# Performance work log

Measured on AMD Instinct MI355X. Metric: run time of the kernel, lower is better.

The kernel has to match this reference:

```python
import jax, jax.numpy as jnp
import numpy as np
import math

L, D, H, B, NT = 4, 512, 8, 128, 512
D_HID = int(D * 4.0 / 3.0)  # 682; linear0 outputs 2*D_HID for reglu
EPS = 1e-5


def layer_norm(x, g, b):
    mu = jnp.mean(x, axis=-1, keepdims=True)
    var = jnp.var(x, axis=-1, keepdims=True)
    return (x - mu) * jax.lax.rsqrt(var + EPS) * g + b


def mha(x_q, x_kv, Wq, bq, Wk, bk, Wv, bv, Wo, bo):
    q = x_q @ Wq.T + bq
    k = x_kv @ Wk.T + bk
    v = x_kv @ Wv.T + bv
    Bq, Sq, _ = q.shape
    Sk = k.shape[1]
    dh = D // H
    q = q.reshape(Bq, Sq, H, dh).transpose(0, 2, 1, 3)  # [B,H,Sq,dh]
    k = k.reshape(Bq, Sk, H, dh).transpose(0, 2, 1, 3)
    v = v.reshape(Bq, Sk, H, dh).transpose(0, 2, 1, 3)
    dots = jnp.einsum('bhqd,bhkd->bhqk', q, k) / math.sqrt(dh)
    attn = jax.nn.softmax(dots, axis=-1)
    o = jnp.einsum('bhqk,bhkd->bhqd', attn, v)
    o = o.transpose(0, 2, 1, 3).reshape(Bq, Sq, D)
    return o @ Wo.T + bo


def reglu(x):
    a, b = jnp.split(x, 2, axis=-1)
    return a * jax.nn.relu(b)


def setup_inputs() -> dict:
    key = jax.random.key(0)
    ks = iter(jax.random.split(key, 32))
    s = 0.02
    return {
        'x_num': jax.random.normal(next(ks), (B, NT, D), jnp.float32),
        'cls_w': jax.random.normal(next(ks), (1, D), jnp.float32) * s,
        'Wq': jax.random.normal(next(ks), (L, D, D), jnp.float32) * s,
        'bq': jnp.zeros((L, D), jnp.float32),
        'Wk': jax.random.normal(next(ks), (L, D, D), jnp.float32) * s,
        'bk': jnp.zeros((L, D), jnp.float32),
        'Wv': jax.random.normal(next(ks), (L, D, D), jnp.float32) * s,
        'bv': jnp.zeros((L, D), jnp.float32),
        'Wo': jax.random.normal(next(ks), (L, D, D), jnp.float32) * s,
        'bo': jnp.zeros((L, D), jnp.float32),
        'l0_w': jax.random.normal(next(ks), (L, 2 * D_HID, D), jnp.float32) * s,
        'l0_b': jnp.zeros((L, 2 * D_HID), jnp.float32),
        'l1_w': jax.random.normal(next(ks), (L, D, D_HID), jnp.float32) * s,
        'l1_b': jnp.zeros((L, D), jnp.float32),
        'n0_g': jnp.ones((L - 1, D), jnp.float32),
        'n0_b': jnp.zeros((L - 1, D), jnp.float32),
        'n1_g': jnp.ones((L, D), jnp.float32),
        'n1_b': jnp.zeros((L, D), jnp.float32),
        'ln_g': jnp.ones((D,), jnp.float32),
        'ln_b': jnp.zeros((D,), jnp.float32),
        'head_w': jax.random.normal(next(ks), (1, D), jnp.float32) * s,
        'head_b': jnp.zeros((1,), jnp.float32),
    }


def reference(x_num, cls_w, Wq, bq, Wk, bk, Wv, bv, Wo, bo,
              l0_w, l0_b, l1_w, l1_b, n0_g, n0_b, n1_g, n1_b,
              ln_g, ln_b, head_w, head_b):
    # prepend CLS token: cls_weight broadcast over batch
    x_cls = jnp.broadcast_to(cls_w[None], (x_num.shape[0], 1, D))
    x = jnp.concatenate([x_cls, x_num], axis=1)  # [B, NT+1, D]
    for i in range(L):
        is_last = i + 1 == L
        # attention block (prenormalization; layer 0 has no norm0)
        xr = layer_norm(x, n0_g[i - 1], n0_b[i - 1]) if i > 0 else x
        x_q = xr[:, :1] if is_last else xr  # last layer: query only CLS
        xr = mha(x_q, xr, Wq[i], bq[i], Wk[i], bk[i], Wv[i], bv[i], Wo[i], bo[i])
        if is_last:
            x = x[:, :1]
        x = x + xr
        # FFN block with reglu
        xr = layer_norm(x, n1_g[i], n1_b[i])
        xr = reglu(xr @ l0_w[i].T + l0_b[i])
        xr = xr @ l1_w[i].T + l1_b[i]
        x = x + xr
    x = x[:, 0]  # CLS representation [B, D]
    x = layer_norm(x, ln_g, ln_b)
    x = jax.nn.relu(x)
    x = x @ head_w.T + head_b
    return x.squeeze(-1)  # [B]
```

## Files before the change

kernel.cpp:

```cpp
#include <hip/hip_runtime.h>
#include <stdint.h>

typedef __attribute__((ext_vector_type(4))) float f32x4;
typedef __attribute__((ext_vector_type(8))) short short8;
typedef __attribute__((ext_vector_type(8))) _Float16 half8;

#define DMODEL 512
#define SEQ 513
#define BATCH 128
#define NROWS (BATCH*SEQ)
#define DHID 682
#define DHID2 1364
#define HP 768
#define KTRIM 704
#define QKVS 1536
#define KVB 64
#define NKT8 8
#define QSF 0.1803368801111244f

__device__ __forceinline__ float h2f(ushort u){ return (float)__builtin_bit_cast(_Float16, u); }
__device__ __forceinline__ ushort f2h(float f){ return __builtin_bit_cast(ushort, (_Float16)f); }
__device__ __forceinline__ uint pk2h(float a, float b){
  return __builtin_bit_cast(uint, __builtin_amdgcn_cvt_pkrtz(a, b));
}
__device__ __forceinline__ void gload16(const void* g, void* lds){
  __builtin_amdgcn_global_load_lds((const __attribute__((address_space(1))) void*)g,
                                   (__attribute__((address_space(3))) void*)lds, 16, 0, 0);
}
__device__ __forceinline__ int xcd_wg(int orig, int nwg){
  const int q = nwg >> 3, r = nwg & 7;
  const int xcd = orig & 7, idx = orig >> 3;
  return (xcd < r) ? (xcd*(q+1) + idx) : (r*(q+1) + (xcd-r)*q + idx);
}

template<int EPI>
__global__ __launch_bounds__(256,3) void gemm_bt(
    const ushort* __restrict__ A, const ushort* __restrict__ W,
    const float* __restrict__ bias, ushort* __restrict__ Cb, float* __restrict__ Cf,
    int K, int ldc, int gx, int nwg)
{
  __shared__ char lds[32768];
  const int t = threadIdx.x, lane = t & 63, w = t >> 6;
  const int fr = lane & 15, g = lane >> 4;
  const int l7 = lane & 7, l8 = lane >> 3;
  const int wg = xcd_wg(blockIdx.x, nwg);
  const int row0 = (wg / gx) << 7;
  const int col0 = (wg % gx) << 7;
  const int wr = (w >> 1) << 6, wc = (w & 1) << 6;

  const int chunkoff = (l7 ^ l8) << 3;
  const ushort* Ag = A + (size_t)(row0 + w*8 + l8) * K + chunkoff;
  const ushort* Wg = W + (size_t)(col0 + w*8 + l8) * K + chunkoff;

  f32x4 acc[4][4] = {};

  for (int k0 = 0; k0 < K; k0 += 64) {
    __syncthreads();
#pragma unroll
    for (int p = 0; p < 4; ++p) {
      gload16(Ag + (size_t)(p*32)*K + k0, lds + p*4096 + w*1024);
      gload16(Wg + (size_t)(p*32)*K + k0, lds + 16384 + p*4096 + w*1024);
    }
    __syncthreads();
#pragma unroll
    for (int ks = 0; ks < 2; ++ks) {
      half8 af[4], wf[4];
#pragma unroll
      for (int m = 0; m < 4; ++m) {
        const int row = wr + m*16 + fr;
        af[m] = *(const half8*)(lds + row*128 + (((g + ks*4) ^ (fr & 7)) << 4));
      }
#pragma unroll
      for (int n = 0; n < 4; ++n) {
        const int row = wc + n*16 + fr;
        wf[n] = *(const half8*)(lds + 16384 + row*128 + (((g + ks*4) ^ (fr & 7)) << 4));
      }
#pragma unroll
      for (int m = 0; m < 4; ++m)
#pragma unroll
        for (int n = 0; n < 4; ++n)
          acc[m][n] = __builtin_amdgcn_mfma_f32_16x16x32_f16(af[m], wf[n], acc[m][n], 0, 0, 0);
    }
  }

  const int r0 = (lane >> 4) << 2;
#pragma unroll
  for (int m = 0; m < 4; ++m) {
    const int rg = row0 + wr + m*16 + r0;
#pragma unroll
    for (int n = 0; n < 4; ++n) {
      const int cg = col0 + wc + n*16 + fr;
      const float bi = bias[cg];
      if (EPI == 0) {
#pragma unroll
        for (int r = 0; r < 4; ++r)
          Cb[(size_t)(rg + r)*ldc + cg] = f2h(acc[m][n][r] + bi);
      } else {
#pragma unroll
        for (int r = 0; r < 4; ++r) {
          const size_t ix = (size_t)(rg + r)*ldc + cg;
          Cf[ix] += acc[m][n][r] + bi;
        }
      }
    }
  }
}

template<int XW>
__global__ __launch_bounds__(256,2) void gemm_res_ln(
    const ushort* __restrict__ A, const ushort* __restrict__ W,
    const float* __restrict__ bias, float* __restrict__ x,
    const float* __restrict__ gamma, const float* __restrict__ beta,
    ushort* __restrict__ xb, int K, int lda)
{
  __shared__ char lds[73728];
  const int t = threadIdx.x, lane = t & 63, w = t >> 6;
  const int fr = lane & 15, g = lane >> 4;
  const int l7 = lane & 7, l8 = lane >> 3;
  const int row0 = blockIdx.x << 6;

  const int chunkoff = (l7 ^ l8) << 3;
  const ushort* Ag = A + (size_t)(row0 + w*8 + l8) * lda + chunkoff;
  const ushort* Wg = W + (size_t)(w*8 + l8) * lda + chunkoff;

  f32x4 acc[4][8] = {};

  for (int k0 = 0; k0 < K; k0 += 64) {
    __syncthreads();
    gload16(Ag + k0,                   lds + w*1024);
    gload16(Ag + (size_t)32*lda + k0,  lds + 4096 + w*1024);
#pragma unroll
    for (int p = 0; p < 16; ++p)
      gload16(Wg + (size_t)(p*32)*lda + k0, lds + 8192 + p*4096 + w*1024);
    __syncthreads();
#pragma unroll
    for (int ks = 0; ks < 2; ++ks) {
      half8 af[4], wf[8];
#pragma unroll
      for (int m = 0; m < 4; ++m) {
        const int row = m*16 + fr;
        af[m] = *(const half8*)(lds + row*128 + (((g + ks*4) ^ (fr & 7)) << 4));
      }
#pragma unroll
      for (int n = 0; n < 8; ++n) {
        const int row = (w << 7) + n*16 + fr;
        wf[n] = *(const half8*)(lds + 8192 + row*128 + (((g + ks*4) ^ (fr & 7)) << 4));
      }
#pragma unroll
      for (int m = 0; m < 4; ++m)
#pragma unroll
        for (int n = 0; n < 8; ++n)
          acc[m][n] = __builtin_amdgcn_mfma_f32_16x16x32_f16(af[m], wf[n], acc[m][n], 0, 0, 0);
    }
  }

  ushort* fb16   = (ushort*)lds;
  float2* redrow = (float2*)(lds + 66560);
  float*  gb     = (float*)(lds + 67072);

  __syncthreads();
#pragma unroll
  for (int n = 0; n < 8; ++n) {
    const int cg = (w << 7) + n*16 + fr;
    const float bi = bias[cg];
#pragma unroll
    for (int m = 0; m < 4; ++m)
#pragma unroll
      for (int r = 0; r < 4; ++r)
        fb16[(m*16 + g*4 + r)*520 + cg] = f2h(acc[m][n][r] + bi);
  }
  if (t < 128) *(f32x4*)&gb[t*4]            = *(const f32x4*)&gamma[t*4];
  else         *(f32x4*)&gb[512 + (t-128)*4] = *(const f32x4*)&beta[(t-128)*4];
  __syncthreads();

  const int q = t & 15;
  const int rbase = t >> 4;
#pragma unroll
  for (int rr = 0; rr < 4; ++rr) {
    const int row = rr*16 + rbase;
    const int grow = row0 + row;
    const bool wrx = XW || (grow % SEQ) == 0;
    const size_t xrow = (size_t)grow*DMODEL;
    float ps = 0.f, pss = 0.f;
#pragma unroll
    for (int j = 0; j < 8; ++j) {
      const int c = q*4 + j*64;
      const uint2 pk = *(const uint2*)&fb16[row*520 + c];
      f32x4 v;
      v[0] = h2f((ushort)(pk.x & 0xffffu)); v[1] = h2f((ushort)(pk.x >> 16));
      v[2] = h2f((ushort)(pk.y & 0xffffu)); v[3] = h2f((ushort)(pk.y >> 16));
      const f32x4 xo = *(const f32x4*)&x[xrow + c];
      v += xo;
      if (wrx) *(f32x4*)&x[xrow + c] = v;
      uint2 opk; opk.x = pk2h(v[0], v[1]); opk.y = pk2h(v[2], v[3]);
      *(uint2*)&fb16[row*520 + c] = opk;
      ps  += v[0]+v[1]+v[2]+v[3];
      pss += v[0]*v[0]+v[1]*v[1]+v[2]*v[2]+v[3]*v[3];
    }
#pragma unroll
    for (int mask = 1; mask <= 8; mask <<= 1) {
      ps  += __shfl_xor(ps,  mask);
      pss += __shfl_xor(pss, mask);
    }
    if (q == 0) redrow[row] = float2{ps, pss};
  }
  __syncthreads();
#pragma unroll
  for (int rr = 0; rr < 4; ++rr) {
    const int row = rr*16 + rbase;
    const float2 sr = redrow[row];
    const float mu = sr.x * (1.f/512.f);
    const float rstd = rsqrtf(sr.y*(1.f/512.f) - mu*mu + 1e-5f);
    const size_t xbrow = (size_t)(row0 + row)*DMODEL;
#pragma unroll
    for (int j = 0; j < 8; ++j) {
      const int c = q*4 + j*64;
      const uint2 pk = *(const uint2*)&fb16[row*520 + c];
      f32x4 v;
      v[0] = h2f((ushort)(pk.x & 0xffffu)); v[1] = h2f((ushort)(pk.x >> 16));
      v[2] = h2f((ushort)(pk.y & 0xffffu)); v[3] = h2f((ushort)(pk.y >> 16));
      const f32x4 ga = *(const f32x4*)&gb[c];
      const f32x4 be = *(const f32x4*)&gb[512 + c];
      f32x4 o_;
#pragma unroll
      for (int e = 0; e < 4; ++e) o_[e] = (v[e] - mu)*rstd*ga[e] + be[e];
      uint2 u; u.x = pk2h(o_[0], o_[1]); u.y = pk2h(o_[2], o_[3]);
      *(uint2*)&xb[xbrow + c] = u;
    }
  }
}

__global__ __launch_bounds__(256,2) void gemm_ffn(
    const ushort* __restrict__ A, const ushort* __restrict__ Wa, const ushort* __restrict__ Wb,
    const float* __restrict__ ba, const float* __restrict__ bb, ushort* __restrict__ H,
    int K, int ldc, int gx, int nwg)
{
  __shared__ char lds[49152];
  const int t = threadIdx.x, lane = t & 63, w = t >> 6;
  const int fr = lane & 15, g = lane >> 4;
  const int l7 = lane & 7, l8 = lane >> 3;
  const int wg = xcd_wg(blockIdx.x, nwg);
  const int row0 = (wg / gx) << 7;
  const int col0 = (wg % gx) << 7;
  const int wr = (w >> 1) << 6, wc = (w & 1) << 6;

  const int chunkoff = (l7 ^ l8) << 3;
  const ushort* Ag  = A  + (size_t)(row0 + w*8 + l8) * K + chunkoff;
  const ushort* WaG = Wa + (size_t)(col0 + w*8 + l8) * K + chunkoff;
  const ushort* WbG = Wb + (size_t)(col0 + w*8 + l8) * K + chunkoff;

  f32x4 aa[4][4] = {}, ab[4][4] = {};

  for (int k0 = 0; k0 < K; k0 += 64) {
    __syncthreads();
#pragma unroll
    for (int p = 0; p < 4; ++p) {
      gload16(Ag  + (size_t)(p*32)*K + k0, lds + p*4096 + w*1024);
      gload16(WaG + (size_t)(p*32)*K + k0, lds + 16384 + p*4096 + w*1024);
      gload16(WbG + (size_t)(p*32)*K + k0, lds + 32768 + p*4096 + w*1024);
    }
    __syncthreads();
#pragma unroll
    for (int ks = 0; ks < 2; ++ks) {
      half8 af[4], wa[4], wb[4];
#pragma unroll
      for (int m = 0; m < 4; ++m) {
        const int row = wr + m*16 + fr;
        af[m] = *(const half8*)(lds + row*128 + (((g + ks*4) ^ (fr & 7)) << 4));
      }
#pragma unroll
      for (int n = 0; n < 4; ++n) {
        const int row = wc + n*16 + fr;
        const int off = row*128 + (((g + ks*4) ^ (fr & 7)) << 4);
        wa[n] = *(const half8*)(lds + 16384 + off);
        wb[n] = *(const half8*)(lds + 32768 + off);
      }
#pragma unroll
      for (int m = 0; m < 4; ++m)
#pragma unroll
        for (int n = 0; n < 4; ++n) {
          aa[m][n] = __builtin_amdgcn_mfma_f32_16x16x32_f16(af[m], wa[n], aa[m][n], 0, 0, 0);
          ab[m][n] = __builtin_amdgcn_mfma_f32_16x16x32_f16(af[m], wb[n], ab[m][n], 0, 0, 0);
        }
    }
  }

  const int r0 = (lane >> 4) << 2;
#pragma unroll
  for (int m = 0; m < 4; ++m) {
    const int rg = row0 + wr + m*16 + r0;
#pragma unroll
    for (int n = 0; n < 4; ++n) {
      const int cg = col0 + wc + n*16 + fr;
      const float bav = ba[cg], bbv = bb[cg];
#pragma unroll
      for (int r = 0; r < 4; ++r) {
        const float av = aa[m][n][r] + bav;
        const float bv = ab[m][n][r] + bbv;
        H[(size_t)(rg + r)*ldc + cg] = f2h(av * fmaxf(bv, 0.f));
      }
    }
  }
}

__global__ __launch_bounds__(256,4) void attn_fused(
    const ushort* __restrict__ qkv, ushort* __restrict__ o)
{
  __shared__ char lds[40960];
  const int t = threadIdx.x;

  if (blockIdx.x >= 4096) {
    const int bh = blockIdx.x - 4096;
    const int b = bh >> 3, h = bh & 7;
    float* sc   = (float*)lds;
    float* qsh  = (float*)(lds + 2112);
    float* red  = (float*)(lds + 2368);
    float* osum = (float*)(lds + 2432);
    const ushort* k = qkv + 512;
    const ushort* v = qkv + 1024;
    const ushort* qb2 = qkv + (size_t)512*QKVS;
    if (t < 64) qsh[t] = h2f(qb2[(size_t)b*SEQ*QKVS + h*64 + t]);
    __syncthreads();
    for (int key = t; key < SEQ; key += 256) {
      const ushort* kr = k + ((size_t)b*SEQ + key)*QKVS + h*64;
      float s = 0.f;
#pragma unroll
      for (int dv = 0; dv < 8; ++dv) {
        const short8 kv = *(const short8*)(kr + dv*8);
#pragma unroll
        for (int j = 0; j < 8; ++j) s += qsh[dv*8 + j] * h2f((ushort)kv[j]);
      }
      sc[key] = s;
    }
    __syncthreads();
    float lm = -1e30f;
    for (int key = t; key < SEQ; key += 256) lm = fmaxf(lm, sc[key]);
#pragma unroll
    for (int mask=1; mask<64; mask<<=1) lm = fmaxf(lm, __shfl_xor(lm, mask));
    if ((t&63)==0) red[t>>6] = lm;
    __syncthreads();
    const float mx = fmaxf(fmaxf(red[0],red[1]), fmaxf(red[2],red[3]));
    float ls = 0.f;
    for (int key = t; key < SEQ; key += 256){ float pp = exp2f(sc[key]-mx); sc[key]=pp; ls += pp; }
#pragma unroll
    for (int mask=1; mask<64; mask<<=1) ls += __shfl_xor(ls, mask);
    if ((t&63)==0) red[4 + (t>>6)] = ls;
    __syncthreads();
    const float ssum = red[4]+red[5]+red[6]+red[7];
    const int d = t & 63, kc = t >> 6;
    float op = 0.f;
    for (int key = kc; key < SEQ; key += 4)
      op += sc[key] * h2f(v[((size_t)b*SEQ + key)*QKVS + h*64 + d]);
    osum[t] = op;
    __syncthreads();
    if (t < 64) {
      const float oo = (osum[t]+osum[64+t]+osum[128+t]+osum[192+t]) / ssum;
      o[((size_t)b*SEQ + 512)*DMODEL + h*64 + t] = f2h(oo);
    }
    return;
  }

  const int bid = blockIdx.x;
  const int sw = (bid & 7)*512 + (bid >> 3);
  const int qt = sw & 3;
  const int hb = sw >> 2;
  const int h = hb & 7, b = hb >> 3;
  const int lane = t & 63, w = t >> 6;
  const int fr = lane & 15, g = lane >> 4, gq4 = g << 2;
  const size_t rowB = (size_t)b * SEQ;
  const ushort* q = qkv;
  const ushort* k = qkv + 512;
  const ushort* v = qkv + 1024;

  char* const Ks  = lds;
  char* const Vs  = lds + 8192;
  char* const VTs = lds + 16384;
  char* const pb  = lds + 24576 + w*4096;

  const int qr0 = qt*128 + w*32;

  half8 qf[2][2];
#pragma unroll
  for (int nq = 0; nq < 2; ++nq) {
    const int qrow = qr0 + nq*16 + fr;
#pragma unroll
    for (int kk = 0; kk < 2; ++kk)
      qf[nq][kk] = *(const half8*)&q[(rowB + qrow)*QKVS + h*64 + kk*32 + g*8];
  }

  f32x4 accO[2][4];
  float mrun[2], lrun[2];
  {
    const ushort* k512 = k + (rowB + 512)*QKVS + h*64;
    const ushort* v512 = v + (rowB + 512)*QKVS + h*64;
    half8 kf512[2];
#pragma unroll
    for (int kk = 0; kk < 2; ++kk)
      kf512[kk] = *(const half8*)&k512[kk*32 + g*8];
#pragma unroll
    for (int nq = 0; nq < 2; ++nq) {
      float s = 0.f;
#pragma unroll
      for (int kk = 0; kk < 2; ++kk)
#pragma unroll
        for (int j = 0; j < 8; ++j)
          s += (float)qf[nq][kk][j] * (float)kf512[kk][j];
      s += __shfl_xor(s, 16);
      s += __shfl_xor(s, 32);
      mrun[nq] = s;
      lrun[nq] = 1.f;
    }
    float v0[4];
#pragma unroll
    for (int dn = 0; dn < 4; ++dn) v0[dn] = h2f(v512[dn*16 + fr]);
#pragma unroll
    for (int mq = 0; mq < 2; ++mq)
#pragma unroll
      for (int dn = 0; dn < 4; ++dn)
#pragma unroll
        for (int r = 0; r < 4; ++r) accO[mq][dn][r] = v0[dn];
  }

  const int l8 = lane >> 3, l7 = lane & 7;
  const int chunk = l7 ^ l8;
  auto STAGE = [&](int kt2) {
#pragma unroll
    for (int i = 0; i < 2; ++i) {
      const int row = i*32 + (w<<3) + l8;
      const int keyg = kt2*KVB + row;
      const size_t gsrc = (rowB + keyg)*QKVS + h*64 + chunk*8;
      gload16(k + gsrc, Ks + i*4096 + w*1024);
      gload16(v + gsrc, Vs + i*4096 + w*1024);
    }
  };

  const int db  = (lane & 7) | ((w & 1) << 3);
  const int kbq = l8 | ((w & 2) << 2);
  const int d0 = db << 2, key0 = kbq << 2;

  STAGE(0);

  for (int kt = 0; kt < NKT8; ++kt) {
    __syncthreads();

    f32x4 sc4[4][2] = {};
    __builtin_amdgcn_s_setprio(1);
#pragma unroll
    for (int kk = 0; kk < 2; ++kk) {
      half8 kf[4];
#pragma unroll
      for (int mk = 0; mk < 4; ++mk) {
        const int row = mk*16 + fr;
        kf[mk] = *(const half8*)(Ks + row*128 + ((kk*64 + g*16) ^ ((fr&7)<<4)));
      }
#pragma unroll
      for (int mk = 0; mk < 4; ++mk)
#pragma unroll
        for (int nq = 0; nq < 2; ++nq)
          sc4[mk][nq] = __builtin_amdgcn_mfma_f32_16x16x32_f16(kf[mk], qf[nq][kk], sc4[mk][nq], 0, 0, 0);
    }
    __builtin_amdgcn_s_setprio(0);

    {
      uint2 a[4];
#pragma unroll
      for (int i = 0; i < 4; ++i) {
        const int row = key0 + i;
        a[i] = *(const uint2*)(Vs + row*128 + ((d0*2) ^ ((row&7)<<4)));
      }
      uint2 bb[4];
      bb[0].x = (a[0].x & 0xffffu) | (a[1].x << 16);
      bb[0].y = (a[2].x & 0xffffu) | (a[3].x << 16);
      bb[1].x = (a[0].x >> 16) | (a[1].x & 0xffff0000u);
      bb[1].y = (a[2].x >> 16) | (a[3].x & 0xffff0000u);
      bb[2].x = (a[0].y & 0xffffu) | (a[1].y << 16);
      bb[2].y = (a[2].y & 0xffffu) | (a[3].y << 16);
      bb[3].x = (a[0].y >> 16) | (a[1].y & 0xffff0000u);
      bb[3].y = (a[2].y >> 16) | (a[3].y & 0xffff0000u);
#pragma unroll
      for (int j = 0; j < 4; ++j) {
        const int drow = d0 + j;
        *(uint2*)(VTs + drow*128 + ((key0*2) ^ ((drow&7)<<4))) = bb[j];
      }
    }

    __syncthreads();

    if (kt+1 < NKT8) STAGE(kt+1);

    float al2[2];
    bool resc[2];
#pragma unroll
    for (int nq = 0; nq < 2; ++nq) {
      float m0 = fmaxf(fmaxf(sc4[0][nq][0], sc4[0][nq][1]), fmaxf(sc4[0][nq][2], sc4[0][nq][3]));
      float m1 = fmaxf(fmaxf(sc4[1][nq][0], sc4[1][nq][1]), fmaxf(sc4[1][nq][2], sc4[1][nq][3]));
      float m2 = fmaxf(fmaxf(sc4[2][nq][0], sc4[2][nq][1]), fmaxf(sc4[2][nq][2], sc4[2][nq][3]));
      float m3 = fmaxf(fmaxf(sc4[3][nq][0], sc4[3][nq][1]), fmaxf(sc4[3][nq][2], sc4[3][nq][3]));
      float tm = fmaxf(fmaxf(m0, m1), fmaxf(m2, m3));
      tm = fmaxf(tm, __shfl_xor(tm, 16));
      tm = fmaxf(tm, __shfl_xor(tm, 32));
      float mref;
      if (__all(tm - mrun[nq] <= 8.f)) {
        mref = mrun[nq];
        al2[nq] = 1.f; resc[nq] = false;
      } else {
        const float mnew = fmaxf(mrun[nq], tm);
        al2[nq] = exp2f(mrun[nq] - mnew);
        mrun[nq] = mnew;
        mref = mnew;
        resc[nq] = true;
      }
#pragma unroll
      for (int mk = 0; mk < 4; ++mk)
#pragma unroll
        for (int r = 0; r < 4; ++r)
          sc4[mk][nq][r] = exp2f(sc4[mk][nq][r] - mref);
      float r0s = (sc4[0][nq][0] + sc4[0][nq][1]) + (sc4[0][nq][2] + sc4[0][nq][3]);
      float r1s = (sc4[1][nq][0] + sc4[1][nq][1]) + (sc4[1][nq][2] + sc4[1][nq][3]);
      float r2s = (sc4[2][nq][0] + sc4[2][nq][1]) + (sc4[2][nq][2] + sc4[2][nq][3]);
      float r3s = (sc4[3][nq][0] + sc4[3][nq][1]) + (sc4[3][nq][2] + sc4[3][nq][3]);
      float rs = (r0s + r1s) + (r2s + r3s);
      rs += __shfl_xor(rs, 16);
      rs += __shfl_xor(rs, 32);
      lrun[nq] = resc[nq] ? (lrun[nq]*al2[nq] + rs) : (lrun[nq] + rs);
      char* prow = pb + (nq*16 + fr)*128;
#pragma unroll
      for (int mk = 0; mk < 4; ++mk) {
        uint2 pk;
        pk.x = pk2h(sc4[mk][nq][0], sc4[mk][nq][1]);
        pk.y = pk2h(sc4[mk][nq][2], sc4[mk][nq][3]);
        *(uint2*)(prow + ((mk*32 + gq4*2) ^ ((fr&7)<<4))) = pk;
      }
    }

#pragma unroll
    for (int mq = 0; mq < 2; ++mq) {
      if (resc[mq]) {
#pragma unroll
        for (int r = 0; r < 4; ++r) {
          const float alr = __shfl(al2[mq], (lane & 48) | (gq4 + r));
#pragma unroll
          for (int dn = 0; dn < 4; ++dn) accO[mq][dn][r] *= alr;
        }
      }
    }

    asm volatile("" ::: "memory");

    __builtin_amdgcn_s_setprio(1);
#pragma unroll
    for (int kk2 = 0; kk2 < 2; ++kk2) {
      half8 pf[2];
#pragma unroll
      for (int mq = 0; mq < 2; ++mq)
        pf[mq] = *(const half8*)(pb + (mq*16 + fr)*128 + ((kk2*64 + g*16) ^ ((fr&7)<<4)));
      half8 vf[4];
#pragma unroll
      for (int dn = 0; dn < 4; ++dn) {
        const int row = dn*16 + fr;
        vf[dn] = *(const half8*)(VTs + row*128 + ((kk2*64 + g*16) ^ ((fr&7)<<4)));
      }
#pragma unroll
      for (int mq = 0; mq < 2; ++mq)
#pragma unroll
        for (int dn = 0; dn < 4; ++dn)
          accO[mq][dn] = __builtin_amdgcn_mfma_f32_16x16x32_f16(pf[mq], vf[dn], accO[mq][dn], 0, 0, 0);
    }
    __builtin_amdgcn_s_setprio(0);
  }

#pragma unroll
  for (int mq = 0; mq < 2; ++mq)
#pragma unroll
    for (int r = 0; r < 4; ++r) {
      const int qrow = qr0 + mq*16 + gq4 + r;
      const float ls = __shfl(lrun[mq], (lane & 48) | (gq4 + r));
      const float inv = 1.f / ls;
#pragma unroll
      for (int dn = 0; dn < 4; ++dn)
        o[(rowB + qrow)*DMODEL + h*64 + dn*16 + fr] = f2h(accO[mq][dn][r] * inv);
    }
}

__global__ __launch_bounds__(256) void attn_cls(
    const ushort* __restrict__ qbase, size_t qstride,
    const ushort* __restrict__ qkv,
    ushort* __restrict__ obase, size_t ostride)
{
  const int bh = blockIdx.x;
  const int b = bh >> 3, h = bh & 7;
  const int t = threadIdx.x;
  __shared__ float sc[SEQ];
  __shared__ float qsh[64];
  __shared__ float red[8];
  __shared__ float osum[256];
  const ushort* k = qkv + 512;
  const ushort* v = qkv + 1024;
  if (t < 64) qsh[t] = h2f(qbase[(size_t)b*qstride + h*64 + t]);
  __syncthreads();
  for (int key = t; key < SEQ; key += 256) {
    const ushort* kr = k + ((size_t)b*SEQ + key)*QKVS + h*64;
    float s = 0.f;
#pragma unroll
    for (int dv = 0; dv < 8; ++dv) {
      const short8 kv = *(const short8*)(kr + dv*8);
#pragma unroll
      for (int j = 0; j < 8; ++j) s += qsh[dv*8 + j] * h2f((ushort)kv[j]);
    }
    sc[key] = s;
  }
  __syncthreads();
  float lm = -1e30f;
  for (int key = t; key < SEQ; key += 256) lm = fmaxf(lm, sc[key]);
#pragma unroll
  for (int mask=1; mask<64; mask<<=1) lm = fmaxf(lm, __shfl_xor(lm, mask));
  if ((t&63)==0) red[t>>6] = lm;
  __syncthreads();
  const float mx = fmaxf(fmaxf(red[0],red[1]), fmaxf(red[2],red[3]));
  float ls = 0.f;
  for (int key = t; key < SEQ; key += 256){ float pp = exp2f(sc[key]-mx); sc[key]=pp; ls += pp; }
#pragma unroll
  for (int mask=1; mask<64; mask<<=1) ls += __shfl_xor(ls, mask);
  if ((t&63)==0) red[4 + (t>>6)] = ls;
  __syncthreads();
  const float ssum = red[4]+red[5]+red[6]+red[7];
  const int d = t & 63, kc = t >> 6;
  float op = 0.f;
  for (int key = kc; key < SEQ; key += 4)
    op += sc[key] * h2f(v[((size_t)b*SEQ + key)*QKVS + h*64 + d]);
  osum[t] = op;
  __syncthreads();
  if (t < 64) {
    const float oo = (osum[t]+osum[64+t]+osum[128+t]+osum[192+t]) / ssum;
    obase[(size_t)b*ostride + h*64 + t] = f2h(oo);
  }
}

__global__ __launch_bounds__(256) void ln_kernel(
    const float* __restrict__ x, const float* __restrict__ gamma, const float* __restrict__ beta,
    ushort* __restrict__ out, int nrows)
{
  const int row = blockIdx.x*4 + (threadIdx.x >> 6);
  const int lane = threadIdx.x & 63;
  if (row >= nrows) return;
  const float* xr = x + (size_t)row*DMODEL;
  float4 a = *(const float4*)(xr + lane*8);
  float4 b = *(const float4*)(xr + lane*8 + 4);
  float s  = a.x+a.y+a.z+a.w+b.x+b.y+b.z+b.w;
  float ss = a.x*a.x+a.y*a.y+a.z*a.z+a.w*a.w+b.x*b.x+b.y*b.y+b.z*b.z+b.w*b.w;
#pragma unroll
  for (int mask=1; mask<64; mask<<=1){ s += __shfl_xor(s,mask); ss += __shfl_xor(ss,mask); }
  const float mu = s*(1.f/512.f);
  const float rstd = rsqrtf(ss*(1.f/512.f) - mu*mu + 1e-5f);
  float vals[8] = {a.x,a.y,a.z,a.w,b.x,b.y,b.z,b.w};
  short8 pk;
#pragma unroll
  for (int j=0;j<8;++j){
    const int c = lane*8 + j;
    pk[j] = (short)f2h((vals[j]-mu)*rstd*gamma[c] + beta[c]);
  }
  *(short8*)(out + (size_t)row*DMODEL + lane*8) = pk;
}

__global__ void embed_kernel(const float* __restrict__ x_num, const float* __restrict__ cls_w,
                             float* __restrict__ x, ushort* __restrict__ xb)
{
  const size_t i = (size_t)blockIdx.x*256 + threadIdx.x;
  if (i >= (size_t)NROWS*128) return;
  const int row = (int)(i >> 7);
  const int c4 = ((int)(i & 127)) << 2;
  const int b = row / SEQ;
  const int s = row - b*SEQ;
  float4 val;
  if (s == 0) val = *(const float4*)(cls_w + c4);
  else        val = *(const float4*)(x_num + ((size_t)b*512 + (s-1))*512 + c4);
  *(float4*)(x + (size_t)row*DMODEL + c4) = val;
  ushort4 pk;
  pk.x = f2h(val.x); pk.y = f2h(val.y); pk.z = f2h(val.z); pk.w = f2h(val.w);
  *(ushort4*)(xb + (size_t)row*DMODEL + c4) = pk;
}

__global__ void convert_pad(const float* __restrict__ in, ushort* __restrict__ out,
                            int R, int C, int RP, int CP, int layers, float scale,
                            int r0, int srcRL, size_t ostride)
{
  const size_t i = (size_t)blockIdx.x*256 + threadIdx.x;
  const size_t per = (size_t)RP*CP;
  if (i >= per*layers) return;
  const int l = (int)(i / per);
  const int rem = (int)(i - (size_t)l*per);
  const int r = rem / CP;
  const int c = rem - r*CP;
  ushort val = 0;
  if (r < R && c < C) val = f2h(in[((size_t)l*srcRL + r0 + r)*C + c] * scale);
  out[(size_t)l*ostride + (size_t)r*CP + c] = val;
}

__global__ void build_bias(const float* __restrict__ bq, const float* __restrict__ bk,
                           const float* __restrict__ bv, const float* __restrict__ l0b,
                           float* __restrict__ fqkv, float* __restrict__ fa, float* __restrict__ fb)
{
  const int i = blockIdx.x*256 + threadIdx.x;
  if (i < 4*1536) {
    const int l = i / 1536, j = i - l*1536;
    float val;
    if (j < 512)       val = bq[l*512 + j] * QSF;
    else if (j < 1024) val = bk[l*512 + j - 512];
    else               val = bv[l*512 + j - 1024];
    fqkv[i] = val;
  }
  if (i < 4*HP) {
    const int l = i / HP, j = i - l*HP;
    fa[i] = (j < DHID) ? l0b[l*DHID2 + j] : 0.f;
    fb[i] = (j < DHID) ? l0b[l*DHID2 + DHID + j] : 0.f;
  }
}

__global__ void gather_cls(const ushort* __restrict__ xb, const float* __restrict__ x,
                           ushort* __restrict__ xq, float* __restrict__ xc)
{
  const int b = blockIdx.x, lane = threadIdx.x;
  const size_t src = (size_t)b*SEQ*DMODEL;
  *(short8*)(xq + b*DMODEL + lane*8) = *(const short8*)(xb + src + lane*8);
  *(float4*)(xc + b*DMODEL + lane*8)     = *(const float4*)(x + src + lane*8);
  *(float4*)(xc + b*DMODEL + lane*8 + 4) = *(const float4*)(x + src + lane*8 + 4);
}

__global__ void head_kernel(const float* __restrict__ xc, const float* __restrict__ g,
                            const float* __restrict__ be, const float* __restrict__ hw,
                            const float* __restrict__ hb, float* __restrict__ out)
{
  const int row = blockIdx.x;
  const int lane = threadIdx.x;
  const float* xr = xc + (size_t)row*DMODEL;
  float4 a = *(const float4*)(xr + lane*8);
  float4 b = *(const float4*)(xr + lane*8 + 4);
  float s  = a.x+a.y+a.z+a.w+b.x+b.y+b.z+b.w;
  float ss = a.x*a.x+a.y*a.y+a.z*a.z+a.w*a.w+b.x*b.x+b.y*b.y+b.z*b.z+b.w*b.w;
#pragma unroll
  for (int mask=1; mask<64; mask<<=1){ s += __shfl_xor(s,mask); ss += __shfl_xor(ss,mask); }
  const float mu = s*(1.f/512.f);
  const float rstd = rsqrtf(ss*(1.f/512.f) - mu*mu + 1e-5f);
  float vals[8] = {a.x,a.y,a.z,a.w,b.x,b.y,b.z,b.w};
  float acc = 0.f;
#pragma unroll
  for (int j=0;j<8;++j){
    const int c = lane*8 + j;
    float tv = (vals[j]-mu)*rstd*g[c] + be[c];
    acc += fmaxf(tv, 0.f) * hw[c];
  }
#pragma unroll
  for (int mask=1; mask<64; mask<<=1) acc += __shfl_xor(acc, mask);
  if (lane==0) out[row] = acc + hb[0];
}

extern "C" void kernel_launch(void* const* d_in, const int* in_sizes, int n_in,
                              void* d_out, int out_size, void* d_ws, size_t ws_size,
                              hipStream_t stream)
{
  const float* x_num = (const float*)d_in[0];
  const float* cls_w = (const float*)d_in[1];
  const float* Wq = (const float*)d_in[2];
  const float* bq = (const float*)d_in[3];
  const float* Wk = (const float*)d_in[4];
  const float* bk = (const float*)d_in[5];
  const float* Wv = (const float*)d_in[6];
  const float* bv = (const float*)d_in[7];
  const float* Wo = (const float*)d_in[8];
  const float* bo = (const float*)d_in[9];
  const float* l0_w = (const float*)d_in[10];
  const float* l0_b = (const float*)d_in[11];
  const float* l1_w = (const float*)d_in[12];
  const float* l1_b = (const float*)d_in[13];
  const float* n0_g = (const float*)d_in[14];
  const float* n0_b = (const float*)d_in[15];
  const float* n1_g = (const float*)d_in[16];
  const float* n1_b = (const float*)d_in[17];
  const float* ln_g = (const float*)d_in[18];
  const float* ln_b = (const float*)d_in[19];
  const float* head_w = (const float*)d_in[20];
  const float* head_b = (const float*)d_in[21];
  float* out = (float*)d_out;

  char* p = (char*)d_ws;
  auto alloc = [&](size_t bytes){ char* r = p; p += (bytes + 255) & ~(size_t)255; return r; };

  float* x  = (float*)alloc((size_t)NROWS*DMODEL*4);
  char* U   = alloc((size_t)NROWS*DMODEL*2);
  ushort* xb = (ushort*)U;
  ushort* ob = (ushort*)U;
  char* QKVG = alloc((size_t)NROWS*QKVS*2);
  ushort* qkv = (ushort*)QKVG;
  ushort* hbuf = (ushort*)QKVG;
  ushort* wqkvb = (ushort*)alloc((size_t)4*QKVS*512*2);
  ushort* wob  = (ushort*)alloc((size_t)4*512*512*2);
  ushort* wl0a = (ushort*)alloc((size_t)4*HP*512*2);
  ushort* wl0b = (ushort*)alloc((size_t)4*HP*512*2);
  ushort* l1wp = (ushort*)alloc((size_t)4*512*HP*2);
  float*  fqkvb = (float*)alloc((size_t)4*QKVS*4);
  float*  l0ba = (float*)alloc((size_t)4*HP*4);
  float*  l0bb = (float*)alloc((size_t)4*HP*4);
  ushort* xq_cls = (ushort*)alloc(128*512*2);
  float*  xcf = (float*)alloc(128*512*4);
  ushort* qc = (ushort*)alloc(128*512*2);
  ushort* oc = (ushort*)alloc(128*512*2);
  ushort* hc = (ushort*)alloc((size_t)128*HP*2);
  ushort* xcb = (ushort*)alloc(128*512*2);

  auto cdiv = [](size_t a, size_t b){ return (unsigned)((a + b - 1)/b); };

  convert_pad<<<cdiv((size_t)4*512*512,256),256,0,stream>>>(Wq, wqkvb,            512,512,512,512,4, QSF, 0, 512, (size_t)QKVS*512);
  convert_pad<<<cdiv((size_t)4*512*512,256),256,0,stream>>>(Wk, wqkvb + 512*512,  512,512,512,512,4, 1.f, 0, 512, (size_t)QKVS*512);
  convert_pad<<<cdiv((size_t)4*512*512,256),256,0,stream>>>(Wv, wqkvb + 1024*512, 512,512,512,512,4, 1.f, 0, 512, (size_t)QKVS*512);
  convert_pad<<<cdiv((size_t)4*512*512,256),256,0,stream>>>(Wo, wob, 512,512,512,512,4, 1.f, 0, 512, (size_t)512*512);
  convert_pad<<<cdiv((size_t)4*HP*512,256),256,0,stream>>>(l0_w, wl0a, DHID,512,HP,512,4, 1.f, 0,    DHID2, (size_t)HP*512);
  convert_pad<<<cdiv((size_t)4*HP*512,256),256,0,stream>>>(l0_w, wl0b, DHID,512,HP,512,4, 1.f, DHID, DHID2, (size_t)HP*512);
  convert_pad<<<cdiv((size_t)4*512*HP,256),256,0,stream>>>(l1_w, l1wp, 512,DHID,512,HP,4, 1.f, 0, 512, (size_t)512*HP);
  build_bias<<<cdiv(4*QKVS,256),256,0,stream>>>(bq, bk, bv, l0_b, fqkvb, l0ba, l0bb);

  embed_kernel<<<cdiv((size_t)NROWS*128,256),256,0,stream>>>(x_num, cls_w, x, xb);

  const int nwQKV = 12*513, nwF = 6*513, nwKV = 8*513;
  const int nRL = NROWS/64;
  for (int i = 0; i < 3; ++i) {
    gemm_bt<0><<<nwQKV,256,0,stream>>>(xb, wqkvb+(size_t)i*QKVS*512, fqkvb+(size_t)i*QKVS, qkv, nullptr, 512, QKVS, 12, nwQKV);
    attn_fused<<<5120,256,0,stream>>>(qkv, ob);
    gemm_res_ln<1><<<nRL,256,0,stream>>>(ob, wob+(size_t)i*262144, bo+i*512, x,
                                         n1_g+(size_t)i*512, n1_b+(size_t)i*512, xb, 512, 512);
    gemm_ffn<<<nwF,256,0,stream>>>(xb, wl0a+(size_t)i*HP*512, wl0b+(size_t)i*HP*512,
                                   l0ba+(size_t)i*HP, l0bb+(size_t)i*HP, hbuf, 512, HP, 6, nwF);
    if (i < 2)
      gemm_res_ln<1><<<nRL,256,0,stream>>>(hbuf, l1wp+(size_t)i*512*HP, l1_b+i*512, x,
                                           n0_g+(size_t)i*512, n0_b+(size_t)i*512, xb, KTRIM, HP);
    else
      gemm_res_ln<0><<<nRL,256,0,stream>>>(hbuf, l1wp+(size_t)i*512*HP, l1_b+i*512, x,
                                           n0_g+(size_t)i*512, n0_b+(size_t)i*512, xb, KTRIM, HP);
  }

  gather_cls<<<128,64,0,stream>>>(xb, x, xq_cls, xcf);
  gemm_bt<0><<<4,256,0,stream>>>(xq_cls, wqkvb+(size_t)3*QKVS*512, fqkvb+(size_t)3*QKVS, qc, nullptr, 512, 512, 4, 4);
  gemm_bt<0><<<nwKV,256,0,stream>>>(xb, wqkvb+(size_t)3*QKVS*512 + 512*512, fqkvb+(size_t)3*QKVS + 512,
                                    qkv + 512, nullptr, 512, QKVS, 8, nwKV);
  attn_cls<<<1024,256,0,stream>>>(qc, 512, qkv, oc, 512);
  gemm_bt<1><<<4,256,0,stream>>>(oc, wob+(size_t)3*262144, bo+3*512, nullptr, xcf, 512, 512, 4, 4);
  ln_kernel<<<cdiv(128,4),256,0,stream>>>(xcf, n1_g+3*512, n1_b+3*512, xcb, 128);
  gemm_ffn<<<6,256,0,stream>>>(xcb, wl0a+(size_t)3*HP*512, wl0b+(size_t)3*HP*512,
                               l0ba+(size_t)3*HP, l0bb+(size_t)3*HP, hc, 512, HP, 6, 6);
  gemm_bt<1><<<4,256,0,stream>>>(hc, l1wp+(size_t)3*512*HP, l1_b+3*512, nullptr, xcf, HP, 512, 4, 4);
  head_kernel<<<128,64,0,stream>>>(xcf, ln_g, ln_b, head_w, head_b, out);
}
```

Baseline: 2.318 ms.

## Double attention block to 512 threads covering 256 query rows per block

Each attention block grows from 4 to 8 waves and handles 256 query rows instead of 128, so every K/V tile staged into LDS is reused by twice as many queries and the number of query-tile blocks halves. Staging and the V transpose are redistributed so each wave moves half as much data. The CLS-row path's reductions are widened to 8 waves. LDS grows to 56KB per block and the launch bound drops to two blocks per CU, which reduces occupancy and makes each barrier wait on more waves.

```diff
diff --git a/kernel.cpp b/kernel.cpp
--- a/kernel.cpp
+++ b/kernel.cpp
@@ -303,14 +303,14 @@
   }
 }
 
-__global__ __launch_bounds__(256,4) void attn_fused(
+__global__ __launch_bounds__(512,2) void attn_fused(
     const ushort* __restrict__ qkv, ushort* __restrict__ o)
 {
-  __shared__ char lds[40960];
+  __shared__ char lds[57344];
   const int t = threadIdx.x;
 
-  if (blockIdx.x >= 4096) {
-    const int bh = blockIdx.x - 4096;
+  if (blockIdx.x >= 2048) {
+    const int bh = blockIdx.x - 2048;
     const int b = bh >> 3, h = bh & 7;
     float* sc   = (float*)lds;
     float* qsh  = (float*)(lds + 2112);
@@ -321,7 +321,7 @@
     const ushort* qb2 = qkv + (size_t)512*QKVS;
     if (t < 64) qsh[t] = h2f(qb2[(size_t)b*SEQ*QKVS + h*64 + t]);
     __syncthreads();
-    for (int key = t; key < SEQ; key += 256) {
+    for (int key = t; key < SEQ; key += 512) {
       const ushort* kr = k + ((size_t)b*SEQ + key)*QKVS + h*64;
       float s = 0.f;
 #pragma unroll
@@ -334,36 +334,39 @@
     }
     __syncthreads();
     float lm = -1e30f;
-    for (int key = t; key < SEQ; key += 256) lm = fmaxf(lm, sc[key]);
+    for (int key = t; key < SEQ; key += 512) lm = fmaxf(lm, sc[key]);
 #pragma unroll
     for (int mask=1; mask<64; mask<<=1) lm = fmaxf(lm, __shfl_xor(lm, mask));
     if ((t&63)==0) red[t>>6] = lm;
     __syncthreads();
-    const float mx = fmaxf(fmaxf(red[0],red[1]), fmaxf(red[2],red[3]));
+    const float mx = fmaxf(fmaxf(fmaxf(red[0],red[1]), fmaxf(red[2],red[3])),
+                           fmaxf(fmaxf(red[4],red[5]), fmaxf(red[6],red[7])));
     float ls = 0.f;
-    for (int key = t; key < SEQ; key += 256){ float pp = exp2f(sc[key]-mx); sc[key]=pp; ls += pp; }
+    for (int key = t; key < SEQ; key += 512){ float pp = exp2f(sc[key]-mx); sc[key]=pp; ls += pp; }
 #pragma unroll
     for (int mask=1; mask<64; mask<<=1) ls += __shfl_xor(ls, mask);
-    if ((t&63)==0) red[4 + (t>>6)] = ls;
-    __syncthreads();
-    const float ssum = red[4]+red[5]+red[6]+red[7];
+    if ((t&63)==0) red[8 + (t>>6)] = ls;
+    __syncthreads();
+    const float ssum = ((red[8]+red[9]) + (red[10]+red[11]))
+                     + ((red[12]+red[13]) + (red[14]+red[15]));
     const int d = t & 63, kc = t >> 6;
     float op = 0.f;
-    for (int key = kc; key < SEQ; key += 4)
+    for (int key = kc; key < SEQ; key += 8)
       op += sc[key] * h2f(v[((size_t)b*SEQ + key)*QKVS + h*64 + d]);
     osum[t] = op;
     __syncthreads();
     if (t < 64) {
-      const float oo = (osum[t]+osum[64+t]+osum[128+t]+osum[192+t]) / ssum;
+      const float oo = (((osum[t]+osum[64+t]) + (osum[128+t]+osum[192+t]))
+                      + ((osum[256+t]+osum[320+t]) + (osum[384+t]+osum[448+t]))) / ssum;
       o[((size_t)b*SEQ + 512)*DMODEL + h*64 + t] = f2h(oo);
     }
     return;
   }
 
   const int bid = blockIdx.x;
-  const int sw = (bid & 7)*512 + (bid >> 3);
-  const int qt = sw & 3;
-  const int hb = sw >> 2;
+  const int sw = (bid & 7)*256 + (bid >> 3);
+  const int qt2 = sw & 1;
+  const int hb = sw >> 1;
   const int h = hb & 7, b = hb >> 3;
   const int lane = t & 63, w = t >> 6;
   const int fr = lane & 15, g = lane >> 4, gq4 = g << 2;
@@ -377,7 +380,7 @@
   char* const VTs = lds + 16384;
   char* const pb  = lds + 24576 + w*4096;
 
-  const int qr0 = qt*128 + w*32;
+  const int qr0 = qt2*256 + w*32;
 
   half8 qf[2][2];
 #pragma unroll
@@ -424,19 +427,18 @@
   const int l8 = lane >> 3, l7 = lane & 7;
   const int chunk = l7 ^ l8;
   auto STAGE = [&](int kt2) {
-#pragma unroll
-    for (int i = 0; i < 2; ++i) {
-      const int row = i*32 + (w<<3) + l8;
-      const int keyg = kt2*KVB + row;
-      const size_t gsrc = (rowB + keyg)*QKVS + h*64 + chunk*8;
-      gload16(k + gsrc, Ks + i*4096 + w*1024);
-      gload16(v + gsrc, Vs + i*4096 + w*1024);
-    }
+    const int row = (w << 3) + l8;
+    const int keyg = kt2*KVB + row;
+    const size_t gsrc = (rowB + keyg)*QKVS + h*64 + chunk*8;
+    gload16(k + gsrc, Ks + w*1024);
+    gload16(v + gsrc, Vs + w*1024);
   };
 
+  const int dh  = (w >> 1) & 1;
   const int db  = (lane & 7) | ((w & 1) << 3);
-  const int kbq = l8 | ((w & 2) << 2);
+  const int kbq = l8 | ((w & 4) << 1);
   const int d0 = db << 2, key0 = kbq << 2;
+  const int dA = d0 + 2*dh, dB = dA + 1;
 
   STAGE(0);
 
@@ -462,26 +464,19 @@
     __builtin_amdgcn_s_setprio(0);
 
     {
-      uint2 a[4];
+      uint a[4];
 #pragma unroll
       for (int i = 0; i < 4; ++i) {
         const int row = key0 + i;
-        a[i] = *(const uint2*)(Vs + row*128 + ((d0*2) ^ ((row&7)<<4)));
-      }
-      uint2 bb[4];
-      bb[0].x = (a[0].x & 0xffffu) | (a[1].x << 16);
-      bb[0].y = (a[2].x & 0xffffu) | (a[3].x << 16);
-      bb[1].x = (a[0].x >> 16) | (a[1].x & 0xffff0000u);
-      bb[1].y = (a[2].x >> 16) | (a[3].x & 0xffff0000u);
-      bb[2].x = (a[0].y & 0xffffu) | (a[1].y << 16);
-      bb[2].y = (a[2].y & 0xffffu) | (a[3].y << 16);
-      bb[3].x = (a[0].y >> 16) | (a[1].y & 0xffff0000u);
-      bb[3].y = (a[2].y >> 16) | (a[3].y & 0xffff0000u);
-#pragma unroll
-      for (int j = 0; j < 4; ++j) {
-        const int drow = d0 + j;
-        *(uint2*)(VTs + drow*128 + ((key0*2) ^ ((drow&7)<<4))) = bb[j];
-      }
+        a[i] = *(const uint*)(Vs + row*128 + (((dA*2) ^ ((row&7)<<4))));
+      }
+      uint2 b0, b1;
+      b0.x = (a[0] & 0xffffu) | (a[1] << 16);
+      b0.y = (a[2] & 0xffffu) | (a[3] << 16);
+      b1.x = (a[0] >> 16) | (a[1] & 0xffff0000u);
+      b1.y = (a[2] >> 16) | (a[3] & 0xffff0000u);
+      *(uint2*)(VTs + dA*128 + ((key0*2) ^ ((dA&7)<<4))) = b0;
+      *(uint2*)(VTs + dB*128 + ((key0*2) ^ ((dB&7)<<4))) = b1;
     }
 
     __syncthreads();
@@ -824,7 +819,7 @@
   const int nRL = NROWS/64;
   for (int i = 0; i < 3; ++i) {
     gemm_bt<0><<<nwQKV,256,0,stream>>>(xb, wqkvb+(size_t)i*QKVS*512, fqkvb+(size_t)i*QKVS, qkv, nullptr, 512, QKVS, 12, nwQKV);
-    attn_fused<<<5120,256,0,stream>>>(qkv, ob);
+    attn_fused<<<3072,512,0,stream>>>(qkv, ob);
     gemm_res_ln<1><<<nRL,256,0,stream>>>(ob, wob+(size_t)i*262144, bo+i*512, x,
                                          n1_g+(size_t)i*512, n1_b+(size_t)i*512, xb, 512, 512);
     gemm_ffn<<<nwF,256,0,stream>>>(xb, wl0a+(size_t)i*HP*512, wl0b+(size_t)i*HP*512,
```

After: 2.509 ms. 1.08x slower.
